# Kernel tuning notes

Hardware: AMD Instinct MI355X
Metric: run time of the kernel (lower is better)

## Reference

```python
import jax, jax.numpy as jnp
import numpy as np

N = 50000
E_RAND = 800000
F_IN = 128
H = 4          # num_heads
D_HID = 32     # hidden per-head dim
D_OUT = 32     # output per-head dim
NEG_SLOPE_ATTN = 0.2   # DGL GATConv attention leaky_relu
NEG_SLOPE_ACT = 0.01   # F.leaky_relu default activation


def setup_inputs() -> dict:
    key = jax.random.key(0)
    ks = jax.random.split(key, 12)
    x = jax.random.normal(ks[0], (N, F_IN), dtype=jnp.float32)
    src_r = jax.random.randint(ks[1], (E_RAND,), 0, N, dtype=jnp.int32)
    dst_r = jax.random.randint(ks[2], (E_RAND,), 0, N, dtype=jnp.int32)
    loop = jnp.arange(N, dtype=jnp.int32)
    src = jnp.concatenate([src_r, loop])  # add_self_loop
    dst = jnp.concatenate([dst_r, loop])
    sc1 = 1.0 / np.sqrt(F_IN)
    sc2 = 1.0 / np.sqrt(H * D_HID)
    W1 = jax.random.normal(ks[3], (F_IN, H * D_HID), dtype=jnp.float32) * sc1
    al1 = jax.random.normal(ks[4], (H, D_HID), dtype=jnp.float32) * sc1
    ar1 = jax.random.normal(ks[5], (H, D_HID), dtype=jnp.float32) * sc1
    b1 = jnp.zeros((H * D_HID,), dtype=jnp.float32)
    W2 = jax.random.normal(ks[6], (H * D_HID, H * D_OUT), dtype=jnp.float32) * sc2
    al2 = jax.random.normal(ks[7], (H, D_OUT), dtype=jnp.float32) * sc2
    ar2 = jax.random.normal(ks[8], (H, D_OUT), dtype=jnp.float32) * sc2
    b2 = jnp.zeros((H * D_OUT,), dtype=jnp.float32)
    return {"x": x, "src": src, "dst": dst,
            "W1": W1, "al1": al1, "ar1": ar1, "b1": b1,
            "W2": W2, "al2": al2, "ar2": ar2, "b2": b2}


def gat_conv(x, src, dst, W, al, ar, b, act_slope):
    n = x.shape[0]
    h, d = al.shape
    feat = (x @ W).reshape(n, h, d)                 # [N,H,D]
    el = jnp.einsum('nhd,hd->nh', feat, al)         # [N,H]
    er = jnp.einsum('nhd,hd->nh', feat, ar)
    # edge attention score on edge u->v: leaky_relu(el[u] + er[v])
    e = jax.nn.leaky_relu(el[src] + er[dst], NEG_SLOPE_ATTN)  # [E,H]
    # edge softmax over incoming edges of each dst node (self-loops guarantee >=1 edge)
    m = jax.ops.segment_max(e, dst, num_segments=n)           # [N,H]
    ex = jnp.exp(e - m[dst])
    s = jax.ops.segment_sum(ex, dst, num_segments=n)
    a = ex / s[dst]                                           # [E,H]
    # attention-weighted scatter-sum of source features
    out = jax.ops.segment_sum(a[:, :, None] * feat[src], dst, num_segments=n)  # [N,H,D]
    out = out + b.reshape(h, d)
    if act_slope is not None:
        out = jax.nn.leaky_relu(out, act_slope)
    return out.reshape(n, h * d)                    # flatten(1)


def reference(x, src, dst, W1, al1, ar1, b1, W2, al2, ar2, b2):
    h = gat_conv(x, src, dst, W1, al1, ar1, b1, NEG_SLOPE_ACT)
    out = gat_conv(h, src, dst, W2, al2, ar2, b2, None)  # last layer: no activation
    return out
```

## Files before the change

kernel.cpp:

```cpp
#include <hip/hip_runtime.h>
#include <hip/hip_bf16.h>
#include <hip/hip_fp16.h>

#define HEADS 4
#define DHEAD 32
#define FDIM 128
#define BCAP 64
#define RPB 64
#define XPAD (FDIM/4 + 1)
#define BINSH 8
#define MAXBINS 256
#define WSTRIDE 68

typedef float nfloat4 __attribute__((ext_vector_type(4)));

__device__ __forceinline__ void gemm_body(
    const float* __restrict__ X, const float* __restrict__ W,
    const float* __restrict__ al, const float* __restrict__ ar,
    __half* __restrict__ feat, float* __restrict__ el, float* __restrict__ er,
    int n, float* Xs) {
    int r0 = blockIdx.x * RPB;
    int rowsLeft = n - r0; if (rowsLeft > RPB) rowsLeft = RPB;
    {
        nfloat4* xsw = (nfloat4*)Xs;
        const nfloat4* Xg = (const nfloat4*)(X + (size_t)r0 * FDIM);
        for (int i = threadIdx.x; i < RPB * (FDIM / 4); i += 256) {
            int row = i >> 5, c4 = i & 31;
            int sr = row < rowsLeft ? row : 0;
            xsw[row * XPAD + c4] =
                __builtin_nontemporal_load(&Xg[(size_t)sr * (FDIM / 4) + c4]);
        }
    }
    __syncthreads();

    int head = __builtin_amdgcn_readfirstlane(threadIdx.x >> 6);
    int lane = threadIdx.x & 63;
    int row = r0 + lane;
    bool valid = row < n;

    const float4* xs4 = (const float4*)Xs + (size_t)lane * XPAD;
    const float* wb = W + head * DHEAD;

    float acc[32];
#pragma unroll
    for (int j = 0; j < 32; j++) acc[j] = 0.f;

#pragma unroll 4
    for (int k4 = 0; k4 < FDIM / 4; k4++) {
        float4 a = xs4[k4];
#pragma unroll
        for (int kk = 0; kk < 4; kk++) {
            const float4* wr = (const float4*)(wb + (size_t)(k4 * 4 + kk) * FDIM);
            float s = (&a.x)[kk];
#pragma unroll
            for (int j4 = 0; j4 < 8; j4++) {
                float4 wv = wr[j4];
                acc[j4 * 4 + 0] += s * wv.x;
                acc[j4 * 4 + 1] += s * wv.y;
                acc[j4 * 4 + 2] += s * wv.z;
                acc[j4 * 4 + 3] += s * wv.w;
            }
        }
    }

    float elv = 0.f, erv = 0.f;
#pragma unroll
    for (int j = 0; j < 32; j++) {
        elv += acc[j] * al[head * DHEAD + j];
        erv += acc[j] * ar[head * DHEAD + j];
    }
    if (valid) {
        el[(size_t)row * HEADS + head] = elv;
        er[(size_t)row * HEADS + head] = erv;
    }

    if (valid) {
        union { __half2 h2[16]; uint4 u4[4]; } pk;
#pragma unroll
        for (int m = 0; m < 16; m++)
            pk.h2[m] = __floats2half2_rn(acc[2 * m], acc[2 * m + 1]);
        uint4* dstp = (uint4*)(feat + (size_t)row * FDIM + head * DHEAD);
#pragma unroll
        for (int t = 0; t < 4; t++) dstp[t] = pk.u4[t];
    }
}

__global__ __launch_bounds__(256) void k_gemm_l1(
    const float* __restrict__ X, const float* __restrict__ W,
    const float* __restrict__ al, const float* __restrict__ ar,
    __half* __restrict__ feat, float* __restrict__ el, float* __restrict__ er, int n,
    const int* __restrict__ edst, int* __restrict__ bincnt, int E) {
    __shared__ float Xs[RPB * 4 * XPAD];
    __shared__ int hist[MAXBINS];

    for (int i = threadIdx.x; i < MAXBINS; i += 256) hist[i] = 0;
    __syncthreads();
    {
        int nb = gridDim.x;
        int echunk = (E + nb - 1) / nb;
        int e0 = blockIdx.x * echunk;
        int e1 = e0 + echunk; if (e1 > E) e1 = E;
        for (int idx = e0 + threadIdx.x; idx < e1; idx += 256)
            atomicAdd(&hist[__builtin_nontemporal_load(&edst[idx]) >> BINSH], 1);
        __syncthreads();
        int hv = hist[threadIdx.x];
        if (threadIdx.x < MAXBINS && hv) atomicAdd(&bincnt[threadIdx.x], hv);
    }

    gemm_body(X, W, al, ar, feat, el, er, n, Xs);
}

__global__ __launch_bounds__(256) void k_scan(
    const int* __restrict__ bincnt, int* __restrict__ binbase,
    int* __restrict__ cursor, int nbins) {
    __shared__ int sb[MAXBINS];
    int tid = threadIdx.x;
    int v0 = (tid < nbins) ? bincnt[tid] : 0;
    sb[tid] = v0;
    __syncthreads();
    for (int off = 1; off < MAXBINS; off <<= 1) {
        int t = 0;
        if (tid >= off) t = sb[tid - off];
        __syncthreads();
        if (tid >= off) sb[tid] += t;
        __syncthreads();
    }
    int excl = sb[tid] - v0;
    if (tid < nbins) { binbase[tid] = excl; cursor[tid] = excl; }
    if (tid == 0) binbase[nbins] = sb[MAXBINS - 1];
}

__global__ __launch_bounds__(256) void k_p2(
    const int* __restrict__ esrc, const int* __restrict__ edst,
    int* __restrict__ cursor, uint* __restrict__ ebin, int E, int nbins) {
    __shared__ int lcnt[MAXBINS];
    __shared__ int lbase[MAXBINS];
    int tid = threadIdx.x;
    for (int i = tid; i < MAXBINS; i += 256) lcnt[i] = 0;
    __syncthreads();
    int nb = gridDim.x;
    int echunk = (E + nb - 1) / nb;
    int e0 = blockIdx.x * echunk;
    int e1 = e0 + echunk; if (e1 > E) e1 = E;
    int d[5], s[5], lo[5], bb[5];
    bool v[5];
#pragma unroll
    for (int j = 0; j < 5; j++) {
        int idx = e0 + j * 256 + tid;
        v[j] = idx < e1;
        if (v[j]) {
            d[j] = __builtin_nontemporal_load(&edst[idx]);
            s[j] = __builtin_nontemporal_load(&esrc[idx]);
            bb[j] = d[j] >> BINSH;
            lo[j] = atomicAdd(&lcnt[bb[j]], 1);
        }
    }
    __syncthreads();
    if (tid < nbins && lcnt[tid] > 0)
        lbase[tid] = atomicAdd(&cursor[tid], lcnt[tid]);
    __syncthreads();
#pragma unroll
    for (int j = 0; j < 5; j++)
        if (v[j])
            ebin[lbase[bb[j]] + lo[j]] = (uint)(d[j] & 0xffff) | ((uint)s[j] << 16);
}

__global__ __launch_bounds__(256) void k_p3(
    const uint* __restrict__ ebin, const int* __restrict__ binbase,
    ushort* __restrict__ bucket, int* __restrict__ deg, int n) {
    __shared__ int ldeg[MAXBINS];
    int tid = threadIdx.x;
    ldeg[tid] = 0;
    __syncthreads();
    int bin = blockIdx.x;
    int nb0 = bin << BINSH;
    int lo = binbase[bin], hi = binbase[bin + 1];
    for (int i = lo + tid; i < hi; i += 256) {
        uint e = ebin[i];
        int d = (int)(e & 0xffffu);
        int s = (int)(e >> 16);
        int slot = atomicAdd(&ldeg[d - nb0], 1);
        if (slot < BCAP) bucket[((size_t)d << 6) + slot] = (ushort)s;
    }
    __syncthreads();
    int node = nb0 + tid;
    if (node < n) deg[node] = ldeg[tid];
}

__device__ __forceinline__ void agg_body(
    const ushort* __restrict__ bucket, const int* __restrict__ deg,
    const __half2* __restrict__ feat2h, const float* __restrict__ el,
    const float* __restrict__ er, const float* __restrict__ b,
    float* __restrict__ out, int n, int apply_act) {
    __shared__ float ws_all[4][HEADS * WSTRIDE];
    int wave = threadIdx.x >> 6;
    int node = blockIdx.x * 4 + wave;
    if (node >= n) return;
    node = __builtin_amdgcn_readfirstlane(node);
    int lane = threadIdx.x & 63;
    float* ws = ws_all[wave];

    int cnt = __builtin_amdgcn_readfirstlane(deg[node]);
    if (cnt > BCAP) cnt = BCAP;
    const ushort* bkt = bucket + ((size_t)node << 6);

    {
        int ph = lane >> 4;
        int sl = lane & 15;
        float ern = er[(size_t)node * HEADS + ph];
        int slot[4]; float ev[4];
#pragma unroll
        for (int bb = 0; bb < 4; bb++) {
            slot[bb] = bb * 16 + sl;
            int s = (int)bkt[slot[bb]];
            if (s >= n) s = 0;
            ev[bb] = el[(size_t)s * HEADS + ph];
        }
#pragma unroll
        for (int bb = 0; bb < 4; bb++) {
            float t = ev[bb] + ern;
            t = t > 0.f ? t : 0.2f * t;
            float w = (slot[bb] < cnt) ? __expf(t) : 0.f;
            ws[ph * WSTRIDE + slot[bb]] = w;
        }
    }
    asm volatile("s_waitcnt lgkmcnt(0)" ::: "memory");

    int h = lane >> 4;
    const float2* wsh2 = (const float2*)(ws + h * WSTRIDE);
    const uint* bp32 = (const uint*)bkt;
    float ax = 0.f, ay = 0.f, sw = 0.f;
    int pairs = (cnt + 1) >> 1;
    for (int k0 = 0; k0 < pairs; k0 += 4) {
        uint pk[4];
#pragma unroll
        for (int u = 0; u < 4; u++) {
            int kk = k0 + u;
            pk[u] = __builtin_amdgcn_readfirstlane(kk < pairs ? bp32[kk] : 0u);
        }
        __half2 f[8]; float2 w2[4];
#pragma unroll
        for (int u = 0; u < 4; u++) {
            int s0 = (int)(pk[u] & 0xffffu), s1 = (int)(pk[u] >> 16);
            if (s0 >= n) s0 = 0;
            if (s1 >= n) s1 = 0;
            f[2 * u]     = feat2h[(size_t)s0 * 64 + lane];
            f[2 * u + 1] = feat2h[(size_t)s1 * 64 + lane];
            w2[u] = wsh2[k0 + u];
        }
#pragma unroll
        for (int u = 0; u < 4; u++) {
            float2 f0 = __half22float2(f[2 * u]);
            float2 f1 = __half22float2(f[2 * u + 1]);
            sw += w2[u].x + w2[u].y;
            ax += w2[u].x * f0.x + w2[u].y * f1.x;
            ay += w2[u].x * f0.y + w2[u].y * f1.y;
        }
    }

    float inv = 1.0f / sw;
    float2 bv = ((const float2*)b)[lane];
    float ox = ax * inv + bv.x;
    float oy = ay * inv + bv.y;
    if (apply_act) {
        ox = ox > 0.f ? ox : 0.01f * ox;
        oy = oy > 0.f ? oy : 0.01f * oy;
    }
    float2 o; o.x = ox; o.y = oy;
    ((float2*)out)[(size_t)node * 64 + lane] = o;
}

__global__ __launch_bounds__(256) void k_agg_l1(
    const ushort* __restrict__ bucket, const int* __restrict__ deg,
    const __half2* __restrict__ feat2h, const float* __restrict__ el,
    const float* __restrict__ er, const float* __restrict__ b,
    float* __restrict__ out, int n) {
    agg_body(bucket, deg, feat2h, el, er, b, out, n, 1);
}

__global__ __launch_bounds__(256) void k_agg_l2(
    const ushort* __restrict__ bucket, const int* __restrict__ deg,
    const __half2* __restrict__ feat2h, const float* __restrict__ el,
    const float* __restrict__ er, const float* __restrict__ b,
    float* __restrict__ out, int n) {
    agg_body(bucket, deg, feat2h, el, er, b, out, n, 0);
}

__global__ __launch_bounds__(256) void k_gemm_l2(
    const float* __restrict__ X, const float* __restrict__ W,
    const float* __restrict__ al, const float* __restrict__ ar,
    __half* __restrict__ feat, float* __restrict__ el, float* __restrict__ er, int n) {
    __shared__ float Xs[RPB * 4 * XPAD];
    gemm_body(X, W, al, ar, feat, el, er, n, Xs);
}


extern "C" void kernel_launch(void* const* d_in, const int* in_sizes, int n_in,
                              void* d_out, int out_size, void* d_ws, size_t ws_size,
                              hipStream_t stream) {
    const float* x   = (const float*)d_in[0];
    const int*   src = (const int*)d_in[1];
    const int*   dst = (const int*)d_in[2];
    const float* W1  = (const float*)d_in[3];
    const float* al1 = (const float*)d_in[4];
    const float* ar1 = (const float*)d_in[5];
    const float* b1  = (const float*)d_in[6];
    const float* W2  = (const float*)d_in[7];
    const float* al2 = (const float*)d_in[8];
    const float* ar2 = (const float*)d_in[9];
    const float* b2  = (const float*)d_in[10];
    int N = in_sizes[0] / FDIM;
    int E = in_sizes[1];
    float* out = (float*)d_out;

    __half* featA   = (__half*)d_ws;
    float*  elb     = (float*)(featA + (size_t)N * FDIM);
    float*  erb     = elb + (size_t)N * HEADS;
    int*    deg     = (int*)(erb + (size_t)N * HEADS);
    int*    bincnt  = deg + N;
    int*    binbase = bincnt + MAXBINS;
    int*    cursor  = binbase + MAXBINS + 1;
    ushort* bucket  = (ushort*)(cursor + MAXBINS);
    float*  hbuf    = out;
    uint*   ebin    = (uint*)d_out;

    int gblocks = (N + RPB - 1) / RPB;
    int ablocks = (N + 3) / 4;
    int nbins = (N + (1 << BINSH) - 1) >> BINSH;
    int p2b = (E + 1279) / 1280;

    (void)hipMemsetAsync(bincnt, 0, MAXBINS * sizeof(int), stream);

    k_gemm_l1<<<gblocks, 256, 0, stream>>>(x, W1, al1, ar1, featA, elb, erb, N,
                                           dst, bincnt, E);
    k_scan<<<1, 256, 0, stream>>>(bincnt, binbase, cursor, nbins);
    k_p2<<<p2b, 256, 0, stream>>>(src, dst, cursor, ebin, E, nbins);
    k_p3<<<nbins, 256, 0, stream>>>(ebin, binbase, bucket, deg, N);

    k_agg_l1<<<ablocks, 256, 0, stream>>>(bucket, deg, (const __half2*)featA,
                                          elb, erb, b1, hbuf, N);

    k_gemm_l2<<<gblocks, 256, 0, stream>>>(hbuf, W2, al2, ar2, featA, elb, erb, N);
    k_agg_l2<<<ablocks, 256, 0, stream>>>(bucket, deg, (const __half2*)featA,
                                          elb, erb, b2, out, N);
}
```

Baseline: 278.6 us.

## Stage W in LDS, fold scan into binning kernels, replicate bin counters

```diff
diff --git a/kernel.cpp b/kernel.cpp
--- a/kernel.cpp
+++ b/kernel.cpp
@@ -7,47 +7,38 @@
 #define FDIM 128
 #define BCAP 64
 #define RPB 64
-#define XPAD (FDIM/4 + 1)
 #define BINSH 8
 #define MAXBINS 256
+#define NREP 4
 #define WSTRIDE 68
 
-typedef float nfloat4 __attribute__((ext_vector_type(4)));
-
-__device__ __forceinline__ void gemm_body(
-    const float* __restrict__ X, const float* __restrict__ W,
-    const float* __restrict__ al, const float* __restrict__ ar,
-    __half* __restrict__ feat, float* __restrict__ el, float* __restrict__ er,
-    int n, float* Xs) {
-    int r0 = blockIdx.x * RPB;
-    int rowsLeft = n - r0; if (rowsLeft > RPB) rowsLeft = RPB;
-    {
-        nfloat4* xsw = (nfloat4*)Xs;
-        const nfloat4* Xg = (const nfloat4*)(X + (size_t)r0 * FDIM);
-        for (int i = threadIdx.x; i < RPB * (FDIM / 4); i += 256) {
-            int row = i >> 5, c4 = i & 31;
-            int sr = row < rowsLeft ? row : 0;
-            xsw[row * XPAD + c4] =
-                __builtin_nontemporal_load(&Xg[(size_t)sr * (FDIM / 4) + c4]);
-        }
-    }
-    __syncthreads();
-
+__device__ __forceinline__ void stage_W(const float* __restrict__ W, float* Ws) {
+    const float4* Wg = (const float4*)W;
+    float4* Wl = (float4*)Ws;
+    for (int i = threadIdx.x; i < FDIM * FDIM / 4; i += 256)
+        Wl[i] = Wg[i];
+}
+
+__device__ __forceinline__ void gemm_core(
+    const float* __restrict__ X, const float* __restrict__ al,
+    const float* __restrict__ ar, __half* __restrict__ feat,
+    float* __restrict__ el, float* __restrict__ er, int n, const float* Ws) {
     int head = __builtin_amdgcn_readfirstlane(threadIdx.x >> 6);
     int lane = threadIdx.x & 63;
-    int row = r0 + lane;
+    int row = blockIdx.x * RPB + lane;
     bool valid = row < n;
-
-    const float4* xs4 = (const float4*)Xs + (size_t)lane * XPAD;
-    const float* wb = W + head * DHEAD;
+    int cr = valid ? row : (n - 1);
+    const float4* xp = (const float4*)(X + (size_t)cr * FDIM);
+
+    const float* wb = Ws + head * DHEAD;
 
     float acc[32];
 #pragma unroll
     for (int j = 0; j < 32; j++) acc[j] = 0.f;
 
-#pragma unroll 4
+    float4 a = xp[0];
     for (int k4 = 0; k4 < FDIM / 4; k4++) {
-        float4 a = xs4[k4];
+        float4 an = (k4 < FDIM / 4 - 1) ? xp[k4 + 1] : a;
 #pragma unroll
         for (int kk = 0; kk < 4; kk++) {
             const float4* wr = (const float4*)(wb + (size_t)(k4 * 4 + kk) * FDIM);
@@ -61,6 +52,7 @@
                 acc[j4 * 4 + 3] += s * wv.w;
             }
         }
+        a = an;
     }
 
     float elv = 0.f, erv = 0.f;
@@ -90,8 +82,8 @@
     const float* __restrict__ al, const float* __restrict__ ar,
     __half* __restrict__ feat, float* __restrict__ el, float* __restrict__ er, int n,
     const int* __restrict__ edst, int* __restrict__ bincnt, int E) {
-    __shared__ float Xs[RPB * 4 * XPAD];
-    __shared__ int hist[MAXBINS];
+    __shared__ float Ws[FDIM * FDIM];
+    int* hist = (int*)Ws;
 
     for (int i = threadIdx.x; i < MAXBINS; i += 256) hist[i] = 0;
     __syncthreads();
@@ -104,19 +96,38 @@
             atomicAdd(&hist[__builtin_nontemporal_load(&edst[idx]) >> BINSH], 1);
         __syncthreads();
         int hv = hist[threadIdx.x];
-        if (threadIdx.x < MAXBINS && hv) atomicAdd(&bincnt[threadIdx.x], hv);
-    }
-
-    gemm_body(X, W, al, ar, feat, el, er, n, Xs);
-}
-
-__global__ __launch_bounds__(256) void k_scan(
-    const int* __restrict__ bincnt, int* __restrict__ binbase,
-    int* __restrict__ cursor, int nbins) {
+        if (hv) atomicAdd(&bincnt[(blockIdx.x & (NREP - 1)) * MAXBINS + threadIdx.x], hv);
+    }
+    __syncthreads();
+
+    stage_W(W, Ws);
+    __syncthreads();
+    gemm_core(X, al, ar, feat, el, er, n, Ws);
+}
+
+__global__ __launch_bounds__(256) void k_gemm_l2(
+    const float* __restrict__ X, const float* __restrict__ W,
+    const float* __restrict__ al, const float* __restrict__ ar,
+    __half* __restrict__ feat, float* __restrict__ el, float* __restrict__ er, int n) {
+    __shared__ float Ws[FDIM * FDIM];
+    stage_W(W, Ws);
+    __syncthreads();
+    gemm_core(X, al, ar, feat, el, er, n, Ws);
+}
+
+__global__ __launch_bounds__(256) void k_p2(
+    const int* __restrict__ esrc, const int* __restrict__ edst,
+    const int* __restrict__ bincnt, int* __restrict__ cursor,
+    uint* __restrict__ ebin, int E, int nbins) {
     __shared__ int sb[MAXBINS];
+    __shared__ int lcnt[MAXBINS];
+    __shared__ int lbase[MAXBINS];
     int tid = threadIdx.x;
-    int v0 = (tid < nbins) ? bincnt[tid] : 0;
+    int v0 = 0;
+#pragma unroll
+    for (int r = 0; r < NREP; r++) v0 += bincnt[r * MAXBINS + tid];
     sb[tid] = v0;
+    lcnt[tid] = 0;
     __syncthreads();
     for (int off = 1; off < MAXBINS; off <<= 1) {
         int t = 0;
@@ -125,27 +136,12 @@
         if (tid >= off) sb[tid] += t;
         __syncthreads();
     }
-    int excl = sb[tid] - v0;
-    if (tid < nbins) { binbase[tid] = excl; cursor[tid] = excl; }
-    if (tid == 0) binbase[nbins] = sb[MAXBINS - 1];
-}
-
-__global__ __launch_bounds__(256) void k_p2(
-    const int* __restrict__ esrc, const int* __restrict__ edst,
-    int* __restrict__ cursor, uint* __restrict__ ebin, int E, int nbins) {
-    __shared__ int lcnt[MAXBINS];
-    __shared__ int lbase[MAXBINS];
-    int tid = threadIdx.x;
-    for (int i = tid; i < MAXBINS; i += 256) lcnt[i] = 0;
-    __syncthreads();
-    int nb = gridDim.x;
-    int echunk = (E + nb - 1) / nb;
-    int e0 = blockIdx.x * echunk;
-    int e1 = e0 + echunk; if (e1 > E) e1 = E;
-    int d[5], s[5], lo[5], bb[5];
-    bool v[5];
-#pragma unroll
-    for (int j = 0; j < 5; j++) {
+    int e0 = blockIdx.x * 2560;
+    int e1 = e0 + 2560; if (e1 > E) e1 = E;
+    int d[10], s[10], lo[10], bb[10];
+    bool v[10];
+#pragma unroll
+    for (int j = 0; j < 10; j++) {
         int idx = e0 + j * 256 + tid;
         v[j] = idx < e1;
         if (v[j]) {
@@ -156,31 +152,44 @@
         }
     }
     __syncthreads();
-    if (tid < nbins && lcnt[tid] > 0)
-        lbase[tid] = atomicAdd(&cursor[tid], lcnt[tid]);
-    __syncthreads();
-#pragma unroll
-    for (int j = 0; j < 5; j++)
+    int lc = lcnt[tid];
+    if (tid < nbins && lc > 0)
+        lbase[tid] = (sb[tid] - v0) + atomicAdd(&cursor[tid], lc);
+    __syncthreads();
+#pragma unroll
+    for (int j = 0; j < 10; j++)
         if (v[j])
             ebin[lbase[bb[j]] + lo[j]] = (uint)(d[j] & 0xffff) | ((uint)s[j] << 16);
 }
 
 __global__ __launch_bounds__(256) void k_p3(
-    const uint* __restrict__ ebin, const int* __restrict__ binbase,
+    const uint* __restrict__ ebin, const int* __restrict__ bincnt,
     ushort* __restrict__ bucket, int* __restrict__ deg, int n) {
+    __shared__ int sb[MAXBINS];
     __shared__ int ldeg[MAXBINS];
     int tid = threadIdx.x;
+    int v0 = 0;
+#pragma unroll
+    for (int r = 0; r < NREP; r++) v0 += bincnt[r * MAXBINS + tid];
+    sb[tid] = v0;
     ldeg[tid] = 0;
     __syncthreads();
+    for (int off = 1; off < MAXBINS; off <<= 1) {
+        int t = 0;
+        if (tid >= off) t = sb[tid - off];
+        __syncthreads();
+        if (tid >= off) sb[tid] += t;
+        __syncthreads();
+    }
     int bin = blockIdx.x;
+    int hi = sb[bin];
+    int lo = bin > 0 ? sb[bin - 1] : 0;
     int nb0 = bin << BINSH;
-    int lo = binbase[bin], hi = binbase[bin + 1];
     for (int i = lo + tid; i < hi; i += 256) {
         uint e = ebin[i];
-        int d = (int)(e & 0xffffu);
-        int s = (int)(e >> 16);
-        int slot = atomicAdd(&ldeg[d - nb0], 1);
-        if (slot < BCAP) bucket[((size_t)d << 6) + slot] = (ushort)s;
+        int dn = (int)(e & 0xffffu);
+        int slot = atomicAdd(&ldeg[dn - nb0], 1);
+        if (slot < BCAP) bucket[((size_t)dn << 6) + slot] = (ushort)(e >> 16);
     }
     __syncthreads();
     int node = nb0 + tid;
@@ -284,14 +293,6 @@
     const float* __restrict__ er, const float* __restrict__ b,
     float* __restrict__ out, int n) {
     agg_body(bucket, deg, feat2h, el, er, b, out, n, 0);
-}
-
-__global__ __launch_bounds__(256) void k_gemm_l2(
-    const float* __restrict__ X, const float* __restrict__ W,
-    const float* __restrict__ al, const float* __restrict__ ar,
-    __half* __restrict__ feat, float* __restrict__ el, float* __restrict__ er, int n) {
-    __shared__ float Xs[RPB * 4 * XPAD];
-    gemm_body(X, W, al, ar, feat, el, er, n, Xs);
 }
 
 
@@ -318,8 +319,7 @@
     float*  erb     = elb + (size_t)N * HEADS;
     int*    deg     = (int*)(erb + (size_t)N * HEADS);
     int*    bincnt  = deg + N;
-    int*    binbase = bincnt + MAXBINS;
-    int*    cursor  = binbase + MAXBINS + 1;
+    int*    cursor  = bincnt + NREP * MAXBINS;
     ushort* bucket  = (ushort*)(cursor + MAXBINS);
     float*  hbuf    = out;
     uint*   ebin    = (uint*)d_out;
@@ -327,15 +327,14 @@
     int gblocks = (N + RPB - 1) / RPB;
     int ablocks = (N + 3) / 4;
     int nbins = (N + (1 << BINSH) - 1) >> BINSH;
-    int p2b = (E + 1279) / 1280;
-
-    (void)hipMemsetAsync(bincnt, 0, MAXBINS * sizeof(int), stream);
+    int p2b = (E + 2559) / 2560;
+
+    (void)hipMemsetAsync(bincnt, 0, (NREP + 1) * MAXBINS * sizeof(int), stream);
 
     k_gemm_l1<<<gblocks, 256, 0, stream>>>(x, W1, al1, ar1, featA, elb, erb, N,
                                            dst, bincnt, E);
-    k_scan<<<1, 256, 0, stream>>>(bincnt, binbase, cursor, nbins);
-    k_p2<<<p2b, 256, 0, stream>>>(src, dst, cursor, ebin, E, nbins);
-    k_p3<<<nbins, 256, 0, stream>>>(ebin, binbase, bucket, deg, N);
+    k_p2<<<p2b, 256, 0, stream>>>(src, dst, bincnt, cursor, ebin, E, nbins);
+    k_p3<<<nbins, 256, 0, stream>>>(ebin, bincnt, bucket, deg, N);
 
     k_agg_l1<<<ablocks, 256, 0, stream>>>(bucket, deg, (const __half2*)featA,
                                           elb, erb, b1, hbuf, N);
```

Result: no change. 284.0 us (+1.9%).
